# Kernel optimization log

Hardware: AMD Instinct MI355X
Metric: run time of the kernel (lower is better)

## Reference

```python
import jax, jax.numpy as jnp
import numpy as np

N_NODES = 200000
N_EDGES = 1600000
N_GRAPHS = 2000
IN_DIM, W1_DIM, W2_DIM, N_CLASSES = 8, 64, 12, 2


def setup_inputs() -> dict:
    key = jax.random.key(0)
    ks = jax.random.split(key, 9)
    x = jax.random.normal(ks[0], (N_NODES, IN_DIM), dtype=jnp.float32)
    edge_index = jax.random.randint(ks[1], (2, N_EDGES), 0, N_NODES, dtype=jnp.int64)
    batch_index = jnp.sort(jax.random.randint(ks[2], (N_NODES,), 0, N_GRAPHS, dtype=jnp.int64))
    # Glorot-ish scaled params
    W1 = jax.random.normal(ks[3], (IN_DIM, W1_DIM), dtype=jnp.float32) * (1.0 / np.sqrt(IN_DIM))
    b1 = jnp.zeros((W1_DIM,), dtype=jnp.float32)
    W2 = jax.random.normal(ks[4], (W1_DIM, W2_DIM), dtype=jnp.float32) * (1.0 / np.sqrt(W1_DIM))
    b2 = jnp.zeros((W2_DIM,), dtype=jnp.float32)
    Wl = jax.random.normal(ks[5], (W2_DIM, N_CLASSES), dtype=jnp.float32) * (1.0 / np.sqrt(W2_DIM))
    bl = jnp.zeros((N_CLASSES,), dtype=jnp.float32)
    return {"x": x, "edge_index": edge_index, "batch_index": batch_index,
            "W1": W1, "b1": b1, "W2": W2, "b2": b2, "Wl": Wl, "bl": bl}


def _gcn_conv(x, W, b, src, dst, deg_inv_sqrt, n_nodes):
    # x' = D^{-1/2} (A + I) D^{-1/2} X W + b  (self-loops already in src/dst)
    xw = x @ W                                   # [N, out]
    norm = deg_inv_sqrt[src] * deg_inv_sqrt[dst]  # [E+N]
    msg = xw[src] * norm[:, None]                 # edge-wise gather (memory-bound)
    out = jax.ops.segment_sum(msg, dst, num_segments=n_nodes)
    return out + b


def reference(x, edge_index, batch_index, W1, b1, W2, b2, Wl, bl):
    n = x.shape[0]
    loops = jnp.arange(n, dtype=edge_index.dtype)
    src = jnp.concatenate([edge_index[0], loops])
    dst = jnp.concatenate([edge_index[1], loops])
    # degree (with self-loops) on destination nodes, as in PyG gcn_norm
    deg = jax.ops.segment_sum(jnp.ones_like(dst, dtype=x.dtype), dst, num_segments=n)
    deg_inv_sqrt = jax.lax.rsqrt(deg)  # deg >= 1 due to self-loops
    h = jax.nn.relu(_gcn_conv(x, W1, b1, src, dst, deg_inv_sqrt, n))
    h = jax.nn.relu(_gcn_conv(h, W2, b2, src, dst, deg_inv_sqrt, n))
    pooled = jax.ops.segment_max(h, batch_index, num_segments=N_GRAPHS)  # global_max_pool
    logits = pooled @ Wl + bl
    return jax.nn.log_softmax(logits, axis=1)
```

## Files before the change

kernel.cpp:

```cpp
#include <hip/hip_runtime.h>
#include <hip/hip_fp16.h>
#include <stdint.h>


constexpr int IN_DIM = 8;
constexpr int H1 = 64;
constexpr int H2 = 12;
constexpr int NPB = 256;
constexpr int NBK = 782;
constexpr int CAP = 2560;
constexpr int CHUNK = 2048;
constexpr int SLOTS = 16;

__device__ __forceinline__ void acc_row8(float* acc, int4 rv) {
    const __half2* h = (const __half2*)&rv;
#pragma unroll
    for (int q = 0; q < 4; ++q) {
        float2 f = __half22float2(h[q]);
        acc[2 * q] += f.x; acc[2 * q + 1] += f.y;
    }
}

__global__ void __launch_bounds__(256) k_binA(
        const int* __restrict__ src, const int* __restrict__ dst,
        uint32_t* __restrict__ pairs, int* __restrict__ bcursor, int ne) {
    __shared__ int s_cnt[NBK];
    __shared__ int s_start[NBK];
    __shared__ int s_gb[NBK];
    __shared__ int s_tmp[256];
    __shared__ uint32_t s_img[CHUNK];
    __shared__ uint16_t s_bkt[CHUNK];
    int t = threadIdx.x;
    for (int i = t; i < NBK; i += 256) s_cnt[i] = 0;
    __syncthreads();
    int e0 = blockIdx.x * CHUNK;
    int cntblk = min(CHUNK, ne - e0);
    int rec[8];
#pragma unroll
    for (int i = 0; i < 8; ++i) {
        int e = e0 + i * 256 + t;
        rec[i] = -1;
        if (e < ne) {
            int d = __builtin_nontemporal_load(&dst[e]);
            int b = d >> 8;
            int off = atomicAdd(&s_cnt[b], 1);
            rec[i] = (off << 18) | ((d & 255) << 10) | b;
        }
    }
    __syncthreads();
    int b4 = t * 4;
    int v0 = (b4 < NBK) ? s_cnt[b4] : 0;
    int v1 = (b4 + 1 < NBK) ? s_cnt[b4 + 1] : 0;
    int v2 = (b4 + 2 < NBK) ? s_cnt[b4 + 2] : 0;
    int v3 = (b4 + 3 < NBK) ? s_cnt[b4 + 3] : 0;
    int p1 = v0, p2 = v0 + v1, p3 = v0 + v1 + v2, tot = p3 + v3;
    s_tmp[t] = tot;
    __syncthreads();
    for (int off = 1; off < 256; off <<= 1) {
        int u = (t >= off) ? s_tmp[t - off] : 0;
        __syncthreads();
        s_tmp[t] += u;
        __syncthreads();
    }
    int ex = s_tmp[t] - tot;
    if (b4 < NBK)     s_start[b4] = ex;
    if (b4 + 1 < NBK) s_start[b4 + 1] = ex + p1;
    if (b4 + 2 < NBK) s_start[b4 + 2] = ex + p2;
    if (b4 + 3 < NBK) s_start[b4 + 3] = ex + p3;
    for (int b = t; b < NBK; b += 256) {
        int c = s_cnt[b];
        s_gb[b] = (c > 0) ? atomicAdd(&bcursor[b], c) : 0;
    }
    __syncthreads();
#pragma unroll
    for (int i = 0; i < 8; ++i) {
        if (rec[i] < 0) continue;
        int e = e0 + i * 256 + t;
        int b = rec[i] & 1023;
        int dl = (rec[i] >> 10) & 255;
        int off = rec[i] >> 18;
        int pos = s_start[b] + off;
        s_img[pos] = ((uint32_t)dl << 18) | (uint32_t)__builtin_nontemporal_load(&src[e]);
        s_bkt[pos] = (uint16_t)b;
    }
    __syncthreads();
    for (int i = t; i < cntblk; i += 256) {
        int b = s_bkt[i];
        int goff = s_gb[b] + (i - s_start[b]);
        if (goff < CAP) pairs[(size_t)b * CAP + goff] = s_img[i];
    }
}

__global__ void __launch_bounds__(256) k_binB(
        const uint32_t* __restrict__ pairs, const int* __restrict__ bcursor,
        const float* __restrict__ x, int* __restrict__ csr_pad,
        int* __restrict__ csr_ovf, unsigned int* __restrict__ meta,
        float* __restrict__ dis, __half2* __restrict__ xdh, int n) {
    __shared__ int s_hist[NPB];
    __shared__ int s_start[NPB];
    __shared__ int s_tmp[256];
    __shared__ int s_pad[NPB * SLOTS];
    int b = blockIdx.x;
    int t = threadIdx.x;
    int cnt = min(bcursor[b], CAP);
    const uint32_t* pb = pairs + (size_t)b * CAP;
    s_hist[t] = 0;
    for (int i = t; i < NPB * SLOTS; i += 256) s_pad[i] = n;
    __syncthreads();
    uint32_t rdl[10];
    uint32_t rsx[10];
#pragma unroll
    for (int r = 0; r < 10; ++r) {
        int i = t + r * 256;
        rdl[r] = 0xFFFFFFFFu;
        if (i < cnt) {
            uint32_t p = __builtin_nontemporal_load(&pb[i]);
            int dl = (int)(p >> 18);
            int off = atomicAdd(&s_hist[dl], 1);
            rdl[r] = ((uint32_t)off << 8) | (uint32_t)dl;
            rsx[r] = p & 0x3FFFFu;
        }
    }
    __syncthreads();
    int v = s_hist[t];
    s_tmp[t] = v;
    __syncthreads();
    for (int off = 1; off < 256; off <<= 1) {
        int u = (t >= off) ? s_tmp[t - off] : 0;
        __syncthreads();
        s_tmp[t] += u;
        __syncthreads();
    }
    s_start[t] = s_tmp[t] - v;
    __syncthreads();
    int cb = b * CAP;
    int node = (b << 8) + t;
    if (node < n) {
        int deg = s_hist[t];
        meta[node] = ((unsigned int)deg << 21) | (unsigned int)(cb + s_start[t]);
        float di = rsqrtf((float)(deg + 1));
        dis[node] = di;
        const float4* xi = (const float4*)(x + (size_t)node * IN_DIM);
        float4 a = xi[0], c = xi[1];
        union { __half2 h[4]; int iv[4]; } u;
        u.h[0] = __float22half2_rn(make_float2(a.x * di, a.y * di));
        u.h[1] = __float22half2_rn(make_float2(a.z * di, a.w * di));
        u.h[2] = __float22half2_rn(make_float2(c.x * di, c.y * di));
        u.h[3] = __float22half2_rn(make_float2(c.z * di, c.w * di));
        ((int4*)xdh)[node] = make_int4(u.iv[0], u.iv[1], u.iv[2], u.iv[3]);
    } else if (node == n) {
        ((int4*)xdh)[n] = make_int4(0, 0, 0, 0);
    }
#pragma unroll
    for (int r = 0; r < 10; ++r) {
        if (rdl[r] == 0xFFFFFFFFu) continue;
        int dl = (int)(rdl[r] & 255u);
        int pos = (int)(rdl[r] >> 8);
        int sidx = (int)rsx[r];
        if (pos < SLOTS) s_pad[dl * SLOTS + pos] = sidx;
        else             csr_ovf[cb + s_start[dl] + pos] = sidx;
    }
    __syncthreads();
    for (int i = t; i < NPB * SLOTS / 4; i += 256) {
        int node2 = (b << 8) + (i >> 2);
        if (node2 < n)
            ((int4*)csr_pad)[(size_t)(b << 8) * 4 + i] = ((int4*)s_pad)[i];
    }
}

__global__ void __launch_bounds__(256) k_agg1f(
        const int* __restrict__ csr_pad, const int* __restrict__ csr_ovf,
        const unsigned int* __restrict__ meta, const __half2* __restrict__ xdh,
        const float* __restrict__ dis, const float* __restrict__ W1,
        const float* __restrict__ b1, const float* __restrict__ W2,
        __half2* __restrict__ y2h, int n) {
    int node = blockIdx.x * 256 + threadIdx.x;
    if (node > n) return;
    int4* orow = (int4*)y2h + (size_t)node * 2;
    if (node == n) {
        orow[0] = make_int4(0, 0, 0, 0);
        orow[1] = make_int4(0, 0, 0, 0);
        return;
    }
    const int4* pr = (const int4*)(csr_pad + (size_t)node * SLOTS);
    int4 p0 = pr[0], p1 = pr[1], p2 = pr[2], p3 = pr[3];
    unsigned int m = meta[node];
    const int4* xt = (const int4*)xdh;

    float acc[8] = {0, 0, 0, 0, 0, 0, 0, 0};
    int idx[16] = {p0.x, p0.y, p0.z, p0.w, p1.x, p1.y, p1.z, p1.w,
                   p2.x, p2.y, p2.z, p2.w, p3.x, p3.y, p3.z, p3.w};
    acc_row8(acc, xt[node]);
#pragma unroll
    for (int i = 0; i < 16; ++i) acc_row8(acc, xt[(size_t)idx[i]]);
    int deg = m >> 21;
    if (deg > SLOTS) {
        int r0 = (int)(m & 0x1FFFFF);
        for (int r = SLOTS; r < deg; ++r) acc_row8(acc, xt[(size_t)csr_ovf[r0 + r]]);
    }
    float di = dis[node];
    float z[8];
#pragma unroll
    for (int k = 0; k < 8; ++k) z[k] = acc[k] * di;

    float y2[H2];
#pragma unroll
    for (int j = 0; j < H2; ++j) y2[j] = 0.f;
    for (int d = 0; d < H1; ++d) {
        float h = b1[d];
#pragma unroll
        for (int k = 0; k < 8; ++k) h = fmaf(z[k], W1[k * H1 + d], h);
        h = fmaxf(h, 0.f);
#pragma unroll
        for (int j = 0; j < H2; ++j) y2[j] = fmaf(h, W2[d * H2 + j], y2[j]);
    }
    union { __half2 h2v[8]; int iv[8]; } u;
#pragma unroll
    for (int q = 0; q < 6; ++q)
        u.h2v[q] = __float22half2_rn(make_float2(y2[2 * q] * di, y2[2 * q + 1] * di));
    u.h2v[6] = __float22half2_rn(make_float2(0.f, 0.f));
    u.h2v[7] = u.h2v[6];
    orow[0] = make_int4(u.iv[0], u.iv[1], u.iv[2], u.iv[3]);
    orow[1] = make_int4(u.iv[4], u.iv[5], u.iv[6], u.iv[7]);
}

__global__ void __launch_bounds__(256) k_agg2(
        const int* __restrict__ csr_pad, const int* __restrict__ csr_ovf,
        const unsigned int* __restrict__ meta, const __half2* __restrict__ y2h,
        const float* __restrict__ dis, const float* __restrict__ b2,
        const int* __restrict__ batch, unsigned int* __restrict__ pooled, int n) {
    int node = blockIdx.x * 256 + threadIdx.x;
    int lane = threadIdx.x & 63;
    bool active = node < n;
    float v[12] = {0, 0, 0, 0, 0, 0, 0, 0, 0, 0, 0, 0};
    int gid = 0x7fffffff;
    if (active) {
        const int4* pr = (const int4*)(csr_pad + (size_t)node * SLOTS);
        int4 p0 = pr[0], p1 = pr[1], p2 = pr[2], p3 = pr[3];
        unsigned int m = meta[node];
        const int4* yt = (const int4*)y2h;
        float acc[12] = {0, 0, 0, 0, 0, 0, 0, 0, 0, 0, 0, 0};
        auto addrow = [&](int nb) {
            int4 ra = yt[(size_t)nb * 2];
            int4 rb = yt[(size_t)nb * 2 + 1];
            const __half2* ha = (const __half2*)&ra;
            const __half2* hb = (const __half2*)&rb;
#pragma unroll
            for (int q = 0; q < 4; ++q) {
                float2 f = __half22float2(ha[q]);
                acc[2 * q] += f.x; acc[2 * q + 1] += f.y;
            }
#pragma unroll
            for (int q = 0; q < 2; ++q) {
                float2 f = __half22float2(hb[q]);
                acc[8 + 2 * q] += f.x; acc[9 + 2 * q] += f.y;
            }
        };
        int idx[16] = {p0.x, p0.y, p0.z, p0.w, p1.x, p1.y, p1.z, p1.w,
                       p2.x, p2.y, p2.z, p2.w, p3.x, p3.y, p3.z, p3.w};
        addrow(node);
#pragma unroll
        for (int i = 0; i < 16; ++i) addrow(idx[i]);
        int deg = m >> 21;
        if (deg > SLOTS) {
            int r0 = (int)(m & 0x1FFFFF);
            for (int r = SLOTS; r < deg; ++r) addrow(csr_ovf[r0 + r]);
        }
        float di = dis[node];
#pragma unroll
        for (int q = 0; q < 12; ++q) v[q] = fmaxf(fmaf(acc[q], di, b2[q]), 0.f);
        gid = batch[node];
    }
#pragma unroll
    for (int off = 1; off < 64; off <<= 1) {
        int g2 = __shfl_up(gid, off, 64);
        bool merge = (lane >= off) && (g2 == gid);
#pragma unroll
        for (int q = 0; q < 12; ++q) {
            float tv = __shfl_up(v[q], off, 64);
            if (merge) v[q] = fmaxf(v[q], tv);
        }
    }
    int gnext = __shfl_down(gid, 1, 64);
    bool last = (lane == 63) || (gnext != gid);
    if (last && gid != 0x7fffffff) {
        unsigned int* pp = pooled + (size_t)gid * 12;
#pragma unroll
        for (int q = 0; q < 12; ++q) atomicMax(&pp[q], __float_as_uint(v[q]));
    }
}

__global__ void k_head(const unsigned int* __restrict__ pooled,
                       const float* __restrict__ Wl, const float* __restrict__ bl,
                       float* __restrict__ out, int g) {
    int i = blockIdx.x * 256 + threadIdx.x;
    if (i >= g) return;
    float l0 = bl[0], l1 = bl[1];
#pragma unroll
    for (int k = 0; k < H2; ++k) {
        float pv = __uint_as_float(pooled[(size_t)i * 12 + k]);
        l0 = fmaf(pv, Wl[k * 2 + 0], l0);
        l1 = fmaf(pv, Wl[k * 2 + 1], l1);
    }
    float m = fmaxf(l0, l1);
    float lse = m + logf(expf(l0 - m) + expf(l1 - m));
    out[i * 2 + 0] = l0 - lse;
    out[i * 2 + 1] = l1 - lse;
}

extern "C" void kernel_launch(void* const* d_in, const int* in_sizes, int n_in,
                              void* d_out, int out_size, void* d_ws, size_t ws_size,
                              hipStream_t stream) {
    const float* x   = (const float*)d_in[0];
    const int* ei    = (const int*)d_in[1];
    const int* batch = (const int*)d_in[2];
    const float* W1  = (const float*)d_in[3];
    const float* b1  = (const float*)d_in[4];
    const float* W2  = (const float*)d_in[5];
    const float* b2  = (const float*)d_in[6];
    const float* Wl  = (const float*)d_in[7];
    const float* bl  = (const float*)d_in[8];
    float* out = (float*)d_out;

    const int N = in_sizes[0] / IN_DIM;
    const int E = in_sizes[1] / 2;
    const int G = out_size / 2;
    const int* src = ei;
    const int* dst = ei + E;

    auto cdiv = [](long long a, int b) { return (int)((a + b - 1) / b); };

    char* wp = (char*)d_ws;
    auto carve = [&](size_t bytes) {
        char* p = wp;
        wp += (bytes + 63) & ~(size_t)63;
        return p;
    };
    int*          bcursor = (int*)carve(NBK * 4);
    unsigned int* pooled  = (unsigned int*)carve((size_t)G * H2 * 4);
    unsigned int* meta    = (unsigned int*)carve((size_t)N * 4);
    float*        dis     = (float*)carve((size_t)N * 4);
    __half2*      xdh     = (__half2*)carve((size_t)(N + 1) * 16);
    __half2*      y2h     = (__half2*)carve((size_t)(N + 1) * 32);
    uint32_t*     pairs   = (uint32_t*)carve((size_t)NBK * CAP * 4);
    int*          csr_pad = (int*)carve((size_t)N * SLOTS * 4);
    int*          csr_ovf = (int*)carve((size_t)NBK * CAP * 4);

    size_t zspan = (char*)(pooled + (size_t)G * H2) - (char*)bcursor;
    (void)hipMemsetAsync(bcursor, 0, zspan, stream);

    k_binA<<<cdiv(E, CHUNK), 256, 0, stream>>>(src, dst, pairs, bcursor, E);
    k_binB<<<NBK, 256, 0, stream>>>(pairs, bcursor, x, csr_pad, csr_ovf,
                                    meta, dis, xdh, N);

    k_agg1f<<<cdiv((long long)N + 1, 256), 256, 0, stream>>>(
        csr_pad, csr_ovf, meta, xdh, dis, W1, b1, W2, y2h, N);
    k_agg2<<<cdiv(N, 256), 256, 0, stream>>>(csr_pad, csr_ovf, meta, y2h, dis, b2,
                                             batch, pooled, N);
    k_head<<<cdiv(G, 256), 256, 0, stream>>>(pooled, Wl, bl, out, G);
}
```

Baseline: 175.7 us.

## Merge five kernels into two cooperative kernels with grid-wide syncs

Folds the two CSR-binning kernels into one cooperative kernel and the two aggregation kernels plus the head into another. Stage boundaries become grid-wide barriers, and blocks loop persistently over tiles with a grid sized from occupancy queries. The goal is to cut kernel launch overhead and the gaps between launches. The cost is grid-sync latency, a smaller persistent grid that may hide memory latency less well, and a union of shared memory that can lower occupancy.

```diff
diff --git a/kernel.cpp b/kernel.cpp
--- a/kernel.cpp
+++ b/kernel.cpp
@@ -1,6 +1,9 @@
 #include <hip/hip_runtime.h>
 #include <hip/hip_fp16.h>
+#include <hip/hip_cooperative_groups.h>
 #include <stdint.h>
+
+namespace cg = cooperative_groups;
 
 
 constexpr int IN_DIM = 8;
@@ -21,291 +24,305 @@
     }
 }
 
-__global__ void __launch_bounds__(256) k_binA(
+__global__ void __launch_bounds__(256) k_csr(
         const int* __restrict__ src, const int* __restrict__ dst,
-        uint32_t* __restrict__ pairs, int* __restrict__ bcursor, int ne) {
-    __shared__ int s_cnt[NBK];
-    __shared__ int s_start[NBK];
-    __shared__ int s_gb[NBK];
-    __shared__ int s_tmp[256];
-    __shared__ uint32_t s_img[CHUNK];
-    __shared__ uint16_t s_bkt[CHUNK];
-    int t = threadIdx.x;
-    for (int i = t; i < NBK; i += 256) s_cnt[i] = 0;
-    __syncthreads();
-    int e0 = blockIdx.x * CHUNK;
-    int cntblk = min(CHUNK, ne - e0);
-    int rec[8];
-#pragma unroll
-    for (int i = 0; i < 8; ++i) {
-        int e = e0 + i * 256 + t;
-        rec[i] = -1;
-        if (e < ne) {
-            int d = __builtin_nontemporal_load(&dst[e]);
-            int b = d >> 8;
-            int off = atomicAdd(&s_cnt[b], 1);
-            rec[i] = (off << 18) | ((d & 255) << 10) | b;
-        }
-    }
-    __syncthreads();
-    int b4 = t * 4;
-    int v0 = (b4 < NBK) ? s_cnt[b4] : 0;
-    int v1 = (b4 + 1 < NBK) ? s_cnt[b4 + 1] : 0;
-    int v2 = (b4 + 2 < NBK) ? s_cnt[b4 + 2] : 0;
-    int v3 = (b4 + 3 < NBK) ? s_cnt[b4 + 3] : 0;
-    int p1 = v0, p2 = v0 + v1, p3 = v0 + v1 + v2, tot = p3 + v3;
-    s_tmp[t] = tot;
-    __syncthreads();
-    for (int off = 1; off < 256; off <<= 1) {
-        int u = (t >= off) ? s_tmp[t - off] : 0;
-        __syncthreads();
-        s_tmp[t] += u;
-        __syncthreads();
-    }
-    int ex = s_tmp[t] - tot;
-    if (b4 < NBK)     s_start[b4] = ex;
-    if (b4 + 1 < NBK) s_start[b4 + 1] = ex + p1;
-    if (b4 + 2 < NBK) s_start[b4 + 2] = ex + p2;
-    if (b4 + 3 < NBK) s_start[b4 + 3] = ex + p3;
-    for (int b = t; b < NBK; b += 256) {
-        int c = s_cnt[b];
-        s_gb[b] = (c > 0) ? atomicAdd(&bcursor[b], c) : 0;
-    }
-    __syncthreads();
-#pragma unroll
-    for (int i = 0; i < 8; ++i) {
-        if (rec[i] < 0) continue;
-        int e = e0 + i * 256 + t;
-        int b = rec[i] & 1023;
-        int dl = (rec[i] >> 10) & 255;
-        int off = rec[i] >> 18;
-        int pos = s_start[b] + off;
-        s_img[pos] = ((uint32_t)dl << 18) | (uint32_t)__builtin_nontemporal_load(&src[e]);
-        s_bkt[pos] = (uint16_t)b;
-    }
-    __syncthreads();
-    for (int i = t; i < cntblk; i += 256) {
-        int b = s_bkt[i];
-        int goff = s_gb[b] + (i - s_start[b]);
-        if (goff < CAP) pairs[(size_t)b * CAP + goff] = s_img[i];
-    }
-}
-
-__global__ void __launch_bounds__(256) k_binB(
-        const uint32_t* __restrict__ pairs, const int* __restrict__ bcursor,
+        uint32_t* __restrict__ pairs, int* __restrict__ bcursor,
         const float* __restrict__ x, int* __restrict__ csr_pad,
         int* __restrict__ csr_ovf, unsigned int* __restrict__ meta,
-        float* __restrict__ dis, __half2* __restrict__ xdh, int n) {
-    __shared__ int s_hist[NPB];
-    __shared__ int s_start[NPB];
-    __shared__ int s_tmp[256];
-    __shared__ int s_pad[NPB * SLOTS];
-    int b = blockIdx.x;
+        float* __restrict__ dis, __half2* __restrict__ xdh,
+        int ne, int n) {
+    __shared__ union {
+        struct {
+            int cnt[NBK]; int start[NBK]; int gb[NBK]; int tmp[256];
+            uint32_t img[CHUNK]; uint16_t bkt[CHUNK];
+        } A;
+        struct {
+            int hist[NPB]; int start[NPB]; int tmp[256]; int pad[NPB * SLOTS];
+        } B;
+    } S;
     int t = threadIdx.x;
-    int cnt = min(bcursor[b], CAP);
-    const uint32_t* pb = pairs + (size_t)b * CAP;
-    s_hist[t] = 0;
-    for (int i = t; i < NPB * SLOTS; i += 256) s_pad[i] = n;
-    __syncthreads();
-    uint32_t rdl[10];
-    uint32_t rsx[10];
-#pragma unroll
-    for (int r = 0; r < 10; ++r) {
-        int i = t + r * 256;
-        rdl[r] = 0xFFFFFFFFu;
-        if (i < cnt) {
-            uint32_t p = __builtin_nontemporal_load(&pb[i]);
-            int dl = (int)(p >> 18);
-            int off = atomicAdd(&s_hist[dl], 1);
-            rdl[r] = ((uint32_t)off << 8) | (uint32_t)dl;
-            rsx[r] = p & 0x3FFFFu;
-        }
-    }
-    __syncthreads();
-    int v = s_hist[t];
-    s_tmp[t] = v;
-    __syncthreads();
-    for (int off = 1; off < 256; off <<= 1) {
-        int u = (t >= off) ? s_tmp[t - off] : 0;
-        __syncthreads();
-        s_tmp[t] += u;
-        __syncthreads();
-    }
-    s_start[t] = s_tmp[t] - v;
-    __syncthreads();
-    int cb = b * CAP;
-    int node = (b << 8) + t;
-    if (node < n) {
-        int deg = s_hist[t];
-        meta[node] = ((unsigned int)deg << 21) | (unsigned int)(cb + s_start[t]);
-        float di = rsqrtf((float)(deg + 1));
-        dis[node] = di;
-        const float4* xi = (const float4*)(x + (size_t)node * IN_DIM);
-        float4 a = xi[0], c = xi[1];
-        union { __half2 h[4]; int iv[4]; } u;
-        u.h[0] = __float22half2_rn(make_float2(a.x * di, a.y * di));
-        u.h[1] = __float22half2_rn(make_float2(a.z * di, a.w * di));
-        u.h[2] = __float22half2_rn(make_float2(c.x * di, c.y * di));
-        u.h[3] = __float22half2_rn(make_float2(c.z * di, c.w * di));
-        ((int4*)xdh)[node] = make_int4(u.iv[0], u.iv[1], u.iv[2], u.iv[3]);
-    } else if (node == n) {
-        ((int4*)xdh)[n] = make_int4(0, 0, 0, 0);
-    }
-#pragma unroll
-    for (int r = 0; r < 10; ++r) {
-        if (rdl[r] == 0xFFFFFFFFu) continue;
-        int dl = (int)(rdl[r] & 255u);
-        int pos = (int)(rdl[r] >> 8);
-        int sidx = (int)rsx[r];
-        if (pos < SLOTS) s_pad[dl * SLOTS + pos] = sidx;
-        else             csr_ovf[cb + s_start[dl] + pos] = sidx;
-    }
-    __syncthreads();
-    for (int i = t; i < NPB * SLOTS / 4; i += 256) {
-        int node2 = (b << 8) + (i >> 2);
-        if (node2 < n)
-            ((int4*)csr_pad)[(size_t)(b << 8) * 4 + i] = ((int4*)s_pad)[i];
+
+    const int nchunk = (ne + CHUNK - 1) / CHUNK;
+    for (int c = blockIdx.x; c < nchunk; c += gridDim.x) {
+        for (int i = t; i < NBK; i += 256) S.A.cnt[i] = 0;
+        __syncthreads();
+        int e0 = c * CHUNK;
+        int cntblk = min(CHUNK, ne - e0);
+        int rec[8];
+#pragma unroll
+        for (int i = 0; i < 8; ++i) {
+            int e = e0 + i * 256 + t;
+            rec[i] = -1;
+            if (e < ne) {
+                int d = __builtin_nontemporal_load(&dst[e]);
+                int b = d >> 8;
+                int off = atomicAdd(&S.A.cnt[b], 1);
+                rec[i] = (off << 18) | ((d & 255) << 10) | b;
+            }
+        }
+        __syncthreads();
+        int b4 = t * 4;
+        int v0 = (b4 < NBK) ? S.A.cnt[b4] : 0;
+        int v1 = (b4 + 1 < NBK) ? S.A.cnt[b4 + 1] : 0;
+        int v2 = (b4 + 2 < NBK) ? S.A.cnt[b4 + 2] : 0;
+        int v3 = (b4 + 3 < NBK) ? S.A.cnt[b4 + 3] : 0;
+        int p1 = v0, p2 = v0 + v1, p3 = v0 + v1 + v2, tot = p3 + v3;
+        S.A.tmp[t] = tot;
+        __syncthreads();
+        for (int off = 1; off < 256; off <<= 1) {
+            int u = (t >= off) ? S.A.tmp[t - off] : 0;
+            __syncthreads();
+            S.A.tmp[t] += u;
+            __syncthreads();
+        }
+        int ex = S.A.tmp[t] - tot;
+        if (b4 < NBK)     S.A.start[b4] = ex;
+        if (b4 + 1 < NBK) S.A.start[b4 + 1] = ex + p1;
+        if (b4 + 2 < NBK) S.A.start[b4 + 2] = ex + p2;
+        if (b4 + 3 < NBK) S.A.start[b4 + 3] = ex + p3;
+        for (int b = t; b < NBK; b += 256) {
+            int cb = S.A.cnt[b];
+            S.A.gb[b] = (cb > 0) ? atomicAdd(&bcursor[b], cb) : 0;
+        }
+        __syncthreads();
+#pragma unroll
+        for (int i = 0; i < 8; ++i) {
+            if (rec[i] < 0) continue;
+            int e = e0 + i * 256 + t;
+            int b = rec[i] & 1023;
+            int dl = (rec[i] >> 10) & 255;
+            int off = rec[i] >> 18;
+            int pos = S.A.start[b] + off;
+            S.A.img[pos] = ((uint32_t)dl << 18) |
+                           (uint32_t)__builtin_nontemporal_load(&src[e]);
+            S.A.bkt[pos] = (uint16_t)b;
+        }
+        __syncthreads();
+        for (int i = t; i < cntblk; i += 256) {
+            int b = S.A.bkt[i];
+            int goff = S.A.gb[b] + (i - S.A.start[b]);
+            if (goff < CAP) pairs[(size_t)b * CAP + goff] = S.A.img[i];
+        }
+        __syncthreads();
+    }
+
+    __threadfence();
+    cg::this_grid().sync();
+
+    for (int b = blockIdx.x; b < NBK; b += gridDim.x) {
+        int cnt = min(bcursor[b], CAP);
+        const uint32_t* pb = pairs + (size_t)b * CAP;
+        S.B.hist[t] = 0;
+        for (int i = t; i < NPB * SLOTS; i += 256) S.B.pad[i] = n;
+        __syncthreads();
+        uint32_t rdl[10];
+        uint32_t rsx[10];
+#pragma unroll
+        for (int r = 0; r < 10; ++r) {
+            int i = t + r * 256;
+            rdl[r] = 0xFFFFFFFFu;
+            if (i < cnt) {
+                uint32_t p = __builtin_nontemporal_load(&pb[i]);
+                int dl = (int)(p >> 18);
+                int off = atomicAdd(&S.B.hist[dl], 1);
+                rdl[r] = ((uint32_t)off << 8) | (uint32_t)dl;
+                rsx[r] = p & 0x3FFFFu;
+            }
+        }
+        __syncthreads();
+        int v = S.B.hist[t];
+        S.B.tmp[t] = v;
+        __syncthreads();
+        for (int off = 1; off < 256; off <<= 1) {
+            int u = (t >= off) ? S.B.tmp[t - off] : 0;
+            __syncthreads();
+            S.B.tmp[t] += u;
+            __syncthreads();
+        }
+        S.B.start[t] = S.B.tmp[t] - v;
+        __syncthreads();
+        int cb = b * CAP;
+        int node = (b << 8) + t;
+        if (node < n) {
+            int deg = S.B.hist[t];
+            meta[node] = ((unsigned int)deg << 21) | (unsigned int)(cb + S.B.start[t]);
+            float di = rsqrtf((float)(deg + 1));
+            dis[node] = di;
+            const float4* xi = (const float4*)(x + (size_t)node * IN_DIM);
+            float4 a = xi[0], c2 = xi[1];
+            union { __half2 h[4]; int iv[4]; } u;
+            u.h[0] = __float22half2_rn(make_float2(a.x * di, a.y * di));
+            u.h[1] = __float22half2_rn(make_float2(a.z * di, a.w * di));
+            u.h[2] = __float22half2_rn(make_float2(c2.x * di, c2.y * di));
+            u.h[3] = __float22half2_rn(make_float2(c2.z * di, c2.w * di));
+            ((int4*)xdh)[node] = make_int4(u.iv[0], u.iv[1], u.iv[2], u.iv[3]);
+        } else if (node == n) {
+            ((int4*)xdh)[n] = make_int4(0, 0, 0, 0);
+        }
+#pragma unroll
+        for (int r = 0; r < 10; ++r) {
+            if (rdl[r] == 0xFFFFFFFFu) continue;
+            int dl = (int)(rdl[r] & 255u);
+            int pos = (int)(rdl[r] >> 8);
+            int sidx = (int)rsx[r];
+            if (pos < SLOTS) S.B.pad[dl * SLOTS + pos] = sidx;
+            else             csr_ovf[cb + S.B.start[dl] + pos] = sidx;
+        }
+        __syncthreads();
+        for (int i = t; i < NPB * SLOTS / 4; i += 256) {
+            int node2 = (b << 8) + (i >> 2);
+            if (node2 < n)
+                ((int4*)csr_pad)[(size_t)(b << 8) * 4 + i] = ((int4*)S.B.pad)[i];
+        }
+        __syncthreads();
     }
 }
 
-__global__ void __launch_bounds__(256) k_agg1f(
+__global__ void __launch_bounds__(256) k_net(
         const int* __restrict__ csr_pad, const int* __restrict__ csr_ovf,
         const unsigned int* __restrict__ meta, const __half2* __restrict__ xdh,
         const float* __restrict__ dis, const float* __restrict__ W1,
         const float* __restrict__ b1, const float* __restrict__ W2,
-        __half2* __restrict__ y2h, int n) {
-    int node = blockIdx.x * 256 + threadIdx.x;
-    if (node > n) return;
-    int4* orow = (int4*)y2h + (size_t)node * 2;
-    if (node == n) {
-        orow[0] = make_int4(0, 0, 0, 0);
-        orow[1] = make_int4(0, 0, 0, 0);
-        return;
-    }
-    const int4* pr = (const int4*)(csr_pad + (size_t)node * SLOTS);
-    int4 p0 = pr[0], p1 = pr[1], p2 = pr[2], p3 = pr[3];
-    unsigned int m = meta[node];
-    const int4* xt = (const int4*)xdh;
-
-    float acc[8] = {0, 0, 0, 0, 0, 0, 0, 0};
-    int idx[16] = {p0.x, p0.y, p0.z, p0.w, p1.x, p1.y, p1.z, p1.w,
-                   p2.x, p2.y, p2.z, p2.w, p3.x, p3.y, p3.z, p3.w};
-    acc_row8(acc, xt[node]);
-#pragma unroll
-    for (int i = 0; i < 16; ++i) acc_row8(acc, xt[(size_t)idx[i]]);
-    int deg = m >> 21;
-    if (deg > SLOTS) {
-        int r0 = (int)(m & 0x1FFFFF);
-        for (int r = SLOTS; r < deg; ++r) acc_row8(acc, xt[(size_t)csr_ovf[r0 + r]]);
-    }
-    float di = dis[node];
-    float z[8];
-#pragma unroll
-    for (int k = 0; k < 8; ++k) z[k] = acc[k] * di;
-
-    float y2[H2];
-#pragma unroll
-    for (int j = 0; j < H2; ++j) y2[j] = 0.f;
-    for (int d = 0; d < H1; ++d) {
-        float h = b1[d];
-#pragma unroll
-        for (int k = 0; k < 8; ++k) h = fmaf(z[k], W1[k * H1 + d], h);
-        h = fmaxf(h, 0.f);
-#pragma unroll
-        for (int j = 0; j < H2; ++j) y2[j] = fmaf(h, W2[d * H2 + j], y2[j]);
-    }
-    union { __half2 h2v[8]; int iv[8]; } u;
-#pragma unroll
-    for (int q = 0; q < 6; ++q)
-        u.h2v[q] = __float22half2_rn(make_float2(y2[2 * q] * di, y2[2 * q + 1] * di));
-    u.h2v[6] = __float22half2_rn(make_float2(0.f, 0.f));
-    u.h2v[7] = u.h2v[6];
-    orow[0] = make_int4(u.iv[0], u.iv[1], u.iv[2], u.iv[3]);
-    orow[1] = make_int4(u.iv[4], u.iv[5], u.iv[6], u.iv[7]);
-}
-
-__global__ void __launch_bounds__(256) k_agg2(
-        const int* __restrict__ csr_pad, const int* __restrict__ csr_ovf,
-        const unsigned int* __restrict__ meta, const __half2* __restrict__ y2h,
-        const float* __restrict__ dis, const float* __restrict__ b2,
-        const int* __restrict__ batch, unsigned int* __restrict__ pooled, int n) {
-    int node = blockIdx.x * 256 + threadIdx.x;
-    int lane = threadIdx.x & 63;
-    bool active = node < n;
-    float v[12] = {0, 0, 0, 0, 0, 0, 0, 0, 0, 0, 0, 0};
-    int gid = 0x7fffffff;
-    if (active) {
+        __half2* __restrict__ y2h, const float* __restrict__ b2,
+        const int* __restrict__ batch, unsigned int* __restrict__ pooled,
+        const float* __restrict__ Wl, const float* __restrict__ bl,
+        float* __restrict__ out, int n, int g) {
+    int t = threadIdx.x;
+    int lane = t & 63;
+
+    const int nt1 = (n + 1 + 255) / 256;
+    for (int tile = blockIdx.x; tile < nt1; tile += gridDim.x) {
+        int node = tile * 256 + t;
+        if (node > n) continue;
+        int4* orow = (int4*)y2h + (size_t)node * 2;
+        if (node == n) {
+            orow[0] = make_int4(0, 0, 0, 0);
+            orow[1] = make_int4(0, 0, 0, 0);
+            continue;
+        }
         const int4* pr = (const int4*)(csr_pad + (size_t)node * SLOTS);
         int4 p0 = pr[0], p1 = pr[1], p2 = pr[2], p3 = pr[3];
         unsigned int m = meta[node];
-        const int4* yt = (const int4*)y2h;
-        float acc[12] = {0, 0, 0, 0, 0, 0, 0, 0, 0, 0, 0, 0};
-        auto addrow = [&](int nb) {
-            int4 ra = yt[(size_t)nb * 2];
-            int4 rb = yt[(size_t)nb * 2 + 1];
-            const __half2* ha = (const __half2*)&ra;
-            const __half2* hb = (const __half2*)&rb;
-#pragma unroll
-            for (int q = 0; q < 4; ++q) {
-                float2 f = __half22float2(ha[q]);
-                acc[2 * q] += f.x; acc[2 * q + 1] += f.y;
-            }
-#pragma unroll
-            for (int q = 0; q < 2; ++q) {
-                float2 f = __half22float2(hb[q]);
-                acc[8 + 2 * q] += f.x; acc[9 + 2 * q] += f.y;
-            }
-        };
+        const int4* xt = (const int4*)xdh;
+
+        float acc[8] = {0, 0, 0, 0, 0, 0, 0, 0};
         int idx[16] = {p0.x, p0.y, p0.z, p0.w, p1.x, p1.y, p1.z, p1.w,
                        p2.x, p2.y, p2.z, p2.w, p3.x, p3.y, p3.z, p3.w};
-        addrow(node);
-#pragma unroll
-        for (int i = 0; i < 16; ++i) addrow(idx[i]);
+        acc_row8(acc, xt[node]);
+#pragma unroll
+        for (int i = 0; i < 16; ++i) acc_row8(acc, xt[(size_t)idx[i]]);
         int deg = m >> 21;
         if (deg > SLOTS) {
             int r0 = (int)(m & 0x1FFFFF);
-            for (int r = SLOTS; r < deg; ++r) addrow(csr_ovf[r0 + r]);
+            for (int r = SLOTS; r < deg; ++r) acc_row8(acc, xt[(size_t)csr_ovf[r0 + r]]);
         }
         float di = dis[node];
-#pragma unroll
-        for (int q = 0; q < 12; ++q) v[q] = fmaxf(fmaf(acc[q], di, b2[q]), 0.f);
-        gid = batch[node];
-    }
-#pragma unroll
-    for (int off = 1; off < 64; off <<= 1) {
-        int g2 = __shfl_up(gid, off, 64);
-        bool merge = (lane >= off) && (g2 == gid);
-#pragma unroll
-        for (int q = 0; q < 12; ++q) {
-            float tv = __shfl_up(v[q], off, 64);
-            if (merge) v[q] = fmaxf(v[q], tv);
-        }
-    }
-    int gnext = __shfl_down(gid, 1, 64);
-    bool last = (lane == 63) || (gnext != gid);
-    if (last && gid != 0x7fffffff) {
-        unsigned int* pp = pooled + (size_t)gid * 12;
-#pragma unroll
-        for (int q = 0; q < 12; ++q) atomicMax(&pp[q], __float_as_uint(v[q]));
-    }
-}
-
-__global__ void k_head(const unsigned int* __restrict__ pooled,
-                       const float* __restrict__ Wl, const float* __restrict__ bl,
-                       float* __restrict__ out, int g) {
-    int i = blockIdx.x * 256 + threadIdx.x;
-    if (i >= g) return;
-    float l0 = bl[0], l1 = bl[1];
-#pragma unroll
-    for (int k = 0; k < H2; ++k) {
-        float pv = __uint_as_float(pooled[(size_t)i * 12 + k]);
-        l0 = fmaf(pv, Wl[k * 2 + 0], l0);
-        l1 = fmaf(pv, Wl[k * 2 + 1], l1);
-    }
-    float m = fmaxf(l0, l1);
-    float lse = m + logf(expf(l0 - m) + expf(l1 - m));
-    out[i * 2 + 0] = l0 - lse;
-    out[i * 2 + 1] = l1 - lse;
+        float z[8];
+#pragma unroll
+        for (int k = 0; k < 8; ++k) z[k] = acc[k] * di;
+
+        float y2[H2];
+#pragma unroll
+        for (int j = 0; j < H2; ++j) y2[j] = 0.f;
+        for (int d = 0; d < H1; ++d) {
+            float h = b1[d];
+#pragma unroll
+            for (int k = 0; k < 8; ++k) h = fmaf(z[k], W1[k * H1 + d], h);
+            h = fmaxf(h, 0.f);
+#pragma unroll
+            for (int j = 0; j < H2; ++j) y2[j] = fmaf(h, W2[d * H2 + j], y2[j]);
+        }
+        union { __half2 h2v[8]; int iv[8]; } u;
+#pragma unroll
+        for (int q = 0; q < 6; ++q)
+            u.h2v[q] = __float22half2_rn(make_float2(y2[2 * q] * di, y2[2 * q + 1] * di));
+        u.h2v[6] = __float22half2_rn(make_float2(0.f, 0.f));
+        u.h2v[7] = u.h2v[6];
+        orow[0] = make_int4(u.iv[0], u.iv[1], u.iv[2], u.iv[3]);
+        orow[1] = make_int4(u.iv[4], u.iv[5], u.iv[6], u.iv[7]);
+    }
+
+    __threadfence();
+    cg::this_grid().sync();
+
+    const int nt2 = (n + 255) / 256;
+    for (int tile = blockIdx.x; tile < nt2; tile += gridDim.x) {
+        int node = tile * 256 + t;
+        bool active = node < n;
+        float v[12] = {0, 0, 0, 0, 0, 0, 0, 0, 0, 0, 0, 0};
+        int gid = 0x7fffffff;
+        if (active) {
+            const int4* pr = (const int4*)(csr_pad + (size_t)node * SLOTS);
+            int4 p0 = pr[0], p1 = pr[1], p2 = pr[2], p3 = pr[3];
+            unsigned int m = meta[node];
+            const int4* yt = (const int4*)y2h;
+            float acc[12] = {0, 0, 0, 0, 0, 0, 0, 0, 0, 0, 0, 0};
+            auto addrow = [&](int nb) {
+                int4 ra = yt[(size_t)nb * 2];
+                int4 rb = yt[(size_t)nb * 2 + 1];
+                const __half2* ha = (const __half2*)&ra;
+                const __half2* hb = (const __half2*)&rb;
+#pragma unroll
+                for (int q = 0; q < 4; ++q) {
+                    float2 f = __half22float2(ha[q]);
+                    acc[2 * q] += f.x; acc[2 * q + 1] += f.y;
+                }
+#pragma unroll
+                for (int q = 0; q < 2; ++q) {
+                    float2 f = __half22float2(hb[q]);
+                    acc[8 + 2 * q] += f.x; acc[9 + 2 * q] += f.y;
+                }
+            };
+            int idx[16] = {p0.x, p0.y, p0.z, p0.w, p1.x, p1.y, p1.z, p1.w,
+                           p2.x, p2.y, p2.z, p2.w, p3.x, p3.y, p3.z, p3.w};
+            addrow(node);
+#pragma unroll
+            for (int i = 0; i < 16; ++i) addrow(idx[i]);
+            int deg = m >> 21;
+            if (deg > SLOTS) {
+                int r0 = (int)(m & 0x1FFFFF);
+                for (int r = SLOTS; r < deg; ++r) addrow(csr_ovf[r0 + r]);
+            }
+            float di = dis[node];
+#pragma unroll
+            for (int q = 0; q < 12; ++q) v[q] = fmaxf(fmaf(acc[q], di, b2[q]), 0.f);
+            gid = batch[node];
+        }
+#pragma unroll
+        for (int off = 1; off < 64; off <<= 1) {
+            int g2 = __shfl_up(gid, off, 64);
+            bool merge = (lane >= off) && (g2 == gid);
+#pragma unroll
+            for (int q = 0; q < 12; ++q) {
+                float tv = __shfl_up(v[q], off, 64);
+                if (merge) v[q] = fmaxf(v[q], tv);
+            }
+        }
+        int gnext = __shfl_down(gid, 1, 64);
+        bool last = (lane == 63) || (gnext != gid);
+        if (last && gid != 0x7fffffff) {
+            unsigned int* pp = pooled + (size_t)gid * 12;
+#pragma unroll
+            for (int q = 0; q < 12; ++q) atomicMax(&pp[q], __float_as_uint(v[q]));
+        }
+    }
+
+    __threadfence();
+    cg::this_grid().sync();
+
+    for (int i = blockIdx.x * 256 + t; i < g; i += gridDim.x * 256) {
+        float l0 = bl[0], l1 = bl[1];
+#pragma unroll
+        for (int k = 0; k < H2; ++k) {
+            float pv = __uint_as_float(pooled[(size_t)i * 12 + k]);
+            l0 = fmaf(pv, Wl[k * 2 + 0], l0);
+            l1 = fmaf(pv, Wl[k * 2 + 1], l1);
+        }
+        float m = fmaxf(l0, l1);
+        float lse = m + logf(expf(l0 - m) + expf(l1 - m));
+        out[i * 2 + 0] = l0 - lse;
+        out[i * 2 + 1] = l1 - lse;
+    }
 }
 
 extern "C" void kernel_launch(void* const* d_in, const int* in_sizes, int n_in,
@@ -327,8 +344,6 @@
     const int G = out_size / 2;
     const int* src = ei;
     const int* dst = ei + E;
-
-    auto cdiv = [](long long a, int b) { return (int)((a + b - 1) / b); };
 
     char* wp = (char*)d_ws;
     auto carve = [&](size_t bytes) {
@@ -349,13 +364,34 @@
     size_t zspan = (char*)(pooled + (size_t)G * H2) - (char*)bcursor;
     (void)hipMemsetAsync(bcursor, 0, zspan, stream);
 
-    k_binA<<<cdiv(E, CHUNK), 256, 0, stream>>>(src, dst, pairs, bcursor, E);
-    k_binB<<<NBK, 256, 0, stream>>>(pairs, bcursor, x, csr_pad, csr_ovf,
-                                    meta, dis, xdh, N);
-
-    k_agg1f<<<cdiv((long long)N + 1, 256), 256, 0, stream>>>(
-        csr_pad, csr_ovf, meta, xdh, dis, W1, b1, W2, y2h, N);
-    k_agg2<<<cdiv(N, 256), 256, 0, stream>>>(csr_pad, csr_ovf, meta, y2h, dis, b2,
-                                             batch, pooled, N);
-    k_head<<<cdiv(G, 256), 256, 0, stream>>>(pooled, Wl, bl, out, G);
+    static int gA = 0, gB = 0;
+    if (gA == 0) {
+        int mbA = 1, mbB = 1;
+        (void)hipOccupancyMaxActiveBlocksPerMultiprocessor(&mbA, k_csr, 256, 0);
+        (void)hipOccupancyMaxActiveBlocksPerMultiprocessor(&mbB, k_net, 256, 0);
+        if (mbA < 1) mbA = 1;
+        if (mbB < 1) mbB = 1;
+        long long ca = (long long)mbA * 256, cb = (long long)mbB * 256;
+        gA = (int)(ca < NBK ? ca : NBK);
+        gB = (int)(cb < NBK ? cb : NBK);
+    }
+
+    int E_ = E, N_ = N, G_ = G;
+    const int* srcp = src; const int* dstp = dst;
+    const float* xp = x;
+    void* pa[] = {(void*)&srcp, (void*)&dstp, (void*)&pairs, (void*)&bcursor,
+                  (void*)&xp, (void*)&csr_pad, (void*)&csr_ovf, (void*)&meta,
+                  (void*)&dis, (void*)&xdh, (void*)&E_, (void*)&N_};
+    (void)hipLaunchCooperativeKernel((const void*)k_csr, dim3(gA), dim3(256),
+                                     pa, 0, stream);
+
+    const float* W1p = W1; const float* b1p = b1; const float* W2p = W2;
+    const float* b2p = b2; const int* batchp = batch;
+    const float* Wlp = Wl; const float* blp = bl; float* outp = out;
+    void* pb[] = {(void*)&csr_pad, (void*)&csr_ovf, (void*)&meta, (void*)&xdh,
+                  (void*)&dis, (void*)&W1p, (void*)&b1p, (void*)&W2p, (void*)&y2h,
+                  (void*)&b2p, (void*)&batchp, (void*)&pooled, (void*)&Wlp,
+                  (void*)&blp, (void*)&outp, (void*)&N_, (void*)&G_};
+    (void)hipLaunchCooperativeKernel((const void*)k_net, dim3(gB), dim3(256),
+                                     pb, 0, stream);
 }
```

Result: slower. 614.9 us (+250.0%).

## Split layer-2 features into 8+4 planes and aggregate in two passes

Applied to the files above, without the earlier changes.

The 12-channel fp16 layer-2 features were stored as 32-byte padded rows. They are now split into a 16-byte plane (channels 0-7) and an 8-byte plane (channels 8-11). The layer-2 aggregation becomes two kernels, one per plane, so each random gather reads only useful bytes and each table is smaller and more likely to stay in cache. The cost is reading the CSR index lists twice and an extra kernel launch with its own pooling reduction.

```diff
diff --git a/kernel.cpp b/kernel.cpp
--- a/kernel.cpp
+++ b/kernel.cpp
@@ -173,13 +173,12 @@
         const unsigned int* __restrict__ meta, const __half2* __restrict__ xdh,
         const float* __restrict__ dis, const float* __restrict__ W1,
         const float* __restrict__ b1, const float* __restrict__ W2,
-        __half2* __restrict__ y2h, int n) {
+        int4* __restrict__ y2a, int2* __restrict__ y2b, int n) {
     int node = blockIdx.x * 256 + threadIdx.x;
     if (node > n) return;
-    int4* orow = (int4*)y2h + (size_t)node * 2;
     if (node == n) {
-        orow[0] = make_int4(0, 0, 0, 0);
-        orow[1] = make_int4(0, 0, 0, 0);
+        y2a[n] = make_int4(0, 0, 0, 0);
+        y2b[n] = make_int2(0, 0);
         return;
     }
     const int4* pr = (const int4*)(csr_pad + (size_t)node * SLOTS);
@@ -214,61 +213,100 @@
 #pragma unroll
         for (int j = 0; j < H2; ++j) y2[j] = fmaf(h, W2[d * H2 + j], y2[j]);
     }
-    union { __half2 h2v[8]; int iv[8]; } u;
+    union { __half2 h2v[6]; int iv[6]; } u;
 #pragma unroll
     for (int q = 0; q < 6; ++q)
         u.h2v[q] = __float22half2_rn(make_float2(y2[2 * q] * di, y2[2 * q + 1] * di));
-    u.h2v[6] = __float22half2_rn(make_float2(0.f, 0.f));
-    u.h2v[7] = u.h2v[6];
-    orow[0] = make_int4(u.iv[0], u.iv[1], u.iv[2], u.iv[3]);
-    orow[1] = make_int4(u.iv[4], u.iv[5], u.iv[6], u.iv[7]);
-}
-
-__global__ void __launch_bounds__(256) k_agg2(
+    y2a[node] = make_int4(u.iv[0], u.iv[1], u.iv[2], u.iv[3]);
+    y2b[node] = make_int2(u.iv[4], u.iv[5]);
+}
+
+__global__ void __launch_bounds__(256) k_agg2a(
         const int* __restrict__ csr_pad, const int* __restrict__ csr_ovf,
-        const unsigned int* __restrict__ meta, const __half2* __restrict__ y2h,
+        const unsigned int* __restrict__ meta, const int4* __restrict__ y2a,
         const float* __restrict__ dis, const float* __restrict__ b2,
         const int* __restrict__ batch, unsigned int* __restrict__ pooled, int n) {
     int node = blockIdx.x * 256 + threadIdx.x;
     int lane = threadIdx.x & 63;
     bool active = node < n;
-    float v[12] = {0, 0, 0, 0, 0, 0, 0, 0, 0, 0, 0, 0};
+    float v[8] = {0, 0, 0, 0, 0, 0, 0, 0};
     int gid = 0x7fffffff;
     if (active) {
         const int4* pr = (const int4*)(csr_pad + (size_t)node * SLOTS);
         int4 p0 = pr[0], p1 = pr[1], p2 = pr[2], p3 = pr[3];
         unsigned int m = meta[node];
-        const int4* yt = (const int4*)y2h;
-        float acc[12] = {0, 0, 0, 0, 0, 0, 0, 0, 0, 0, 0, 0};
-        auto addrow = [&](int nb) {
-            int4 ra = yt[(size_t)nb * 2];
-            int4 rb = yt[(size_t)nb * 2 + 1];
-            const __half2* ha = (const __half2*)&ra;
-            const __half2* hb = (const __half2*)&rb;
-#pragma unroll
-            for (int q = 0; q < 4; ++q) {
-                float2 f = __half22float2(ha[q]);
+        float acc[8] = {0, 0, 0, 0, 0, 0, 0, 0};
+        int idx[16] = {p0.x, p0.y, p0.z, p0.w, p1.x, p1.y, p1.z, p1.w,
+                       p2.x, p2.y, p2.z, p2.w, p3.x, p3.y, p3.z, p3.w};
+        acc_row8(acc, y2a[node]);
+#pragma unroll
+        for (int i = 0; i < 16; ++i) acc_row8(acc, y2a[(size_t)idx[i]]);
+        int deg = m >> 21;
+        if (deg > SLOTS) {
+            int r0 = (int)(m & 0x1FFFFF);
+            for (int r = SLOTS; r < deg; ++r) acc_row8(acc, y2a[(size_t)csr_ovf[r0 + r]]);
+        }
+        float di = dis[node];
+#pragma unroll
+        for (int q = 0; q < 8; ++q) v[q] = fmaxf(fmaf(acc[q], di, b2[q]), 0.f);
+        gid = batch[node];
+    }
+#pragma unroll
+    for (int off = 1; off < 64; off <<= 1) {
+        int g2 = __shfl_up(gid, off, 64);
+        bool merge = (lane >= off) && (g2 == gid);
+#pragma unroll
+        for (int q = 0; q < 8; ++q) {
+            float tv = __shfl_up(v[q], off, 64);
+            if (merge) v[q] = fmaxf(v[q], tv);
+        }
+    }
+    int gnext = __shfl_down(gid, 1, 64);
+    bool last = (lane == 63) || (gnext != gid);
+    if (last && gid != 0x7fffffff) {
+        unsigned int* pp = pooled + (size_t)gid * 12;
+#pragma unroll
+        for (int q = 0; q < 8; ++q) atomicMax(&pp[q], __float_as_uint(v[q]));
+    }
+}
+
+__global__ void __launch_bounds__(256) k_agg2b(
+        const int* __restrict__ csr_pad, const int* __restrict__ csr_ovf,
+        const unsigned int* __restrict__ meta, const int2* __restrict__ y2b,
+        const float* __restrict__ dis, const float* __restrict__ b2,
+        const int* __restrict__ batch, unsigned int* __restrict__ pooled, int n) {
+    int node = blockIdx.x * 256 + threadIdx.x;
+    int lane = threadIdx.x & 63;
+    bool active = node < n;
+    float v[4] = {0, 0, 0, 0};
+    int gid = 0x7fffffff;
+    if (active) {
+        const int4* pr = (const int4*)(csr_pad + (size_t)node * SLOTS);
+        int4 p0 = pr[0], p1 = pr[1], p2 = pr[2], p3 = pr[3];
+        unsigned int m = meta[node];
+        float acc[4] = {0, 0, 0, 0};
+        auto addrow4 = [&](int nb) {
+            int2 rv = y2b[(size_t)nb];
+            const __half2* h = (const __half2*)&rv;
+#pragma unroll
+            for (int q = 0; q < 2; ++q) {
+                float2 f = __half22float2(h[q]);
                 acc[2 * q] += f.x; acc[2 * q + 1] += f.y;
-            }
-#pragma unroll
-            for (int q = 0; q < 2; ++q) {
-                float2 f = __half22float2(hb[q]);
-                acc[8 + 2 * q] += f.x; acc[9 + 2 * q] += f.y;
             }
         };
         int idx[16] = {p0.x, p0.y, p0.z, p0.w, p1.x, p1.y, p1.z, p1.w,
                        p2.x, p2.y, p2.z, p2.w, p3.x, p3.y, p3.z, p3.w};
-        addrow(node);
-#pragma unroll
-        for (int i = 0; i < 16; ++i) addrow(idx[i]);
+        addrow4(node);
+#pragma unroll
+        for (int i = 0; i < 16; ++i) addrow4(idx[i]);
         int deg = m >> 21;
         if (deg > SLOTS) {
             int r0 = (int)(m & 0x1FFFFF);
-            for (int r = SLOTS; r < deg; ++r) addrow(csr_ovf[r0 + r]);
+            for (int r = SLOTS; r < deg; ++r) addrow4(csr_ovf[r0 + r]);
         }
         float di = dis[node];
 #pragma unroll
-        for (int q = 0; q < 12; ++q) v[q] = fmaxf(fmaf(acc[q], di, b2[q]), 0.f);
+        for (int q = 0; q < 4; ++q) v[q] = fmaxf(fmaf(acc[q], di, b2[8 + q]), 0.f);
         gid = batch[node];
     }
 #pragma unroll
@@ -276,7 +314,7 @@
         int g2 = __shfl_up(gid, off, 64);
         bool merge = (lane >= off) && (g2 == gid);
 #pragma unroll
-        for (int q = 0; q < 12; ++q) {
+        for (int q = 0; q < 4; ++q) {
             float tv = __shfl_up(v[q], off, 64);
             if (merge) v[q] = fmaxf(v[q], tv);
         }
@@ -284,9 +322,9 @@
     int gnext = __shfl_down(gid, 1, 64);
     bool last = (lane == 63) || (gnext != gid);
     if (last && gid != 0x7fffffff) {
-        unsigned int* pp = pooled + (size_t)gid * 12;
-#pragma unroll
-        for (int q = 0; q < 12; ++q) atomicMax(&pp[q], __float_as_uint(v[q]));
+        unsigned int* pp = pooled + (size_t)gid * 12 + 8;
+#pragma unroll
+        for (int q = 0; q < 4; ++q) atomicMax(&pp[q], __float_as_uint(v[q]));
     }
 }
 
@@ -341,7 +379,8 @@
     unsigned int* meta    = (unsigned int*)carve((size_t)N * 4);
     float*        dis     = (float*)carve((size_t)N * 4);
     __half2*      xdh     = (__half2*)carve((size_t)(N + 1) * 16);
-    __half2*      y2h     = (__half2*)carve((size_t)(N + 1) * 32);
+    int4*         y2a     = (int4*)carve((size_t)(N + 1) * 16);
+    int2*         y2b     = (int2*)carve((size_t)(N + 1) * 8);
     uint32_t*     pairs   = (uint32_t*)carve((size_t)NBK * CAP * 4);
     int*          csr_pad = (int*)carve((size_t)N * SLOTS * 4);
     int*          csr_ovf = (int*)carve((size_t)NBK * CAP * 4);
@@ -354,8 +393,10 @@
                                     meta, dis, xdh, N);
 
     k_agg1f<<<cdiv((long long)N + 1, 256), 256, 0, stream>>>(
-        csr_pad, csr_ovf, meta, xdh, dis, W1, b1, W2, y2h, N);
-    k_agg2<<<cdiv(N, 256), 256, 0, stream>>>(csr_pad, csr_ovf, meta, y2h, dis, b2,
-                                             batch, pooled, N);
+        csr_pad, csr_ovf, meta, xdh, dis, W1, b1, W2, y2a, y2b, N);
+    k_agg2a<<<cdiv(N, 256), 256, 0, stream>>>(csr_pad, csr_ovf, meta, y2a,
+                                              dis, b2, batch, pooled, N);
+    k_agg2b<<<cdiv(N, 256), 256, 0, stream>>>(csr_pad, csr_ovf, meta, y2b,
+                                              dis, b2, batch, pooled, N);
     k_head<<<cdiv(G, 256), 256, 0, stream>>>(pooled, Wl, bl, out, G);
 }
```

Measured after the change: 182.2 us. 1.04x slower.
